# Optimization experiments

Measured on AMD Instinct MI355X. Metric: run time of the kernel, lower is better.

## Reference

```python
import jax, jax.numpy as jnp
import numpy as np

NUM_EMBED = 8192
EMBED_DIM = 256


def setup_inputs() -> dict:
    key = jax.random.key(0)
    k1, k2 = jax.random.split(key)
    input_data = jax.random.normal(k1, (32, EMBED_DIM, 32, 32), dtype=jnp.float32)
    codebook = jax.random.normal(k2, (NUM_EMBED, EMBED_DIM), dtype=jnp.float32)
    return {"input_data": input_data, "codebook": codebook}


def reference(input_data, codebook):
    N, C, H, W = input_data.shape
    # NCHW -> NHWC -> [N*H*W, C]
    data = jnp.transpose(input_data, (0, 2, 3, 1)).reshape(-1, C)
    dist = (
        jnp.sum(data * data, axis=1, keepdims=True)          # [T, 1]
        - 2.0 * jnp.einsum("tc,kc->tk", data, codebook)      # [T, K]
        + jnp.sum(codebook * codebook, axis=1)[None, :]       # [1, K]
    )
    embed_ind = jnp.argmin(dist, axis=1)                      # [T]
    quantize = codebook[embed_ind]                            # [T, C] gather
    quantize_detach = data + jax.lax.stop_gradient(quantize - data)
    return quantize, quantize_detach, data
```

## Files before the change

kernel.cpp:

```cpp
#include <hip/hip_runtime.h>
#include <stdint.h>


#define T_TOT 32768
#define K_TOT 8192
#define CD    256
#define SPLITS 4
#define NSPLIT 2048
#define MT    64
#define NTI   32

typedef _Float16 h8 __attribute__((ext_vector_type(8)));
typedef _Float16 h4 __attribute__((ext_vector_type(4)));
typedef float f4 __attribute__((ext_vector_type(4)));
typedef unsigned long long u64;
typedef unsigned int u32;

#define WS_AP    0u
#define WS_BP    16777216u
#define WS_E2    20971520u
#define WS_E2B   21004288u
#define WS_CAND  21037056u
#define WS_NEED  23265280u

__device__ __forceinline__ u64 shfl_xor_u64(u64 v, int off, int w) {
  unsigned lo = (unsigned)v, hi = (unsigned)(v >> 32);
  lo = __shfl_xor(lo, off, w);
  hi = __shfl_xor(hi, off, w);
  return ((u64)hi << 32) | lo;
}
__device__ __forceinline__ u64 umin64(u64 a, u64 b) { return a < b ? a : b; }
__device__ __forceinline__ u64 umax64(u64 a, u64 b) { return a < b ? b : a; }
__device__ __forceinline__ u32 umin32(u32 a, u32 b) { return a < b ? a : b; }
__device__ __forceinline__ u32 umax32(u32 a, u32 b) { return a < b ? b : a; }

__device__ __forceinline__ void gll16(const void* g, void* l) {
  __builtin_amdgcn_global_load_lds(
      (const __attribute__((address_space(1))) void*)g,
      (__attribute__((address_space(3))) void*)l, 16, 0, 0);
}

__device__ __forceinline__ void stage_b(const _Float16* __restrict__ gsrc,
                                        _Float16* ldst, int lane) {
  #pragma unroll
  for (int kk = 0; kk < 8; ++kk)
    gll16(gsrc + kk * 512 + lane * 8, ldst + kk * 512);
}



__global__ __launch_bounds__(256) void cvt_data_kernel(
    const float* __restrict__ in, _Float16* __restrict__ Ap) {
  __shared__ float Ds[32][257];
  const int tid = threadIdx.x;
  const int t0 = blockIdx.x * 32;
  const int nbase = (t0 >> 10) << 18;
  const int tin = t0 & 1023;
  #pragma unroll 8
  for (int p = 0; p < 32; ++p) {
    const int lin = p * 256 + tid;
    const int cc = lin >> 5, tt = lin & 31;
    Ds[tt][cc] = in[nbase + cc * 1024 + tin + tt];
  }
  __syncthreads();
  const u64 g0 = (u64)(t0 >> 4);
  #pragma unroll
  for (int p = 0; p < 4; ++p) {
    const int id = p * 256 + tid;
    const int gl = id >> 9, kk = (id >> 6) & 7, l = id & 63;
    const int row = gl * 16 + (l & 15);
    const int c0 = kk * 32 + (l >> 4) * 8;
    h8 hv;
    #pragma unroll
    for (int j = 0; j < 8; ++j) hv[j] = (_Float16)(-Ds[row][c0 + j]);
    *(h8*)(Ap + ((g0 + (u64)gl) * 8 + kk) * 512 + (u64)l * 8) = hv;
  }
}

__global__ __launch_bounds__(256) void cvt_cb_kernel(
    const float* __restrict__ cb, _Float16* __restrict__ Bp,
    float* __restrict__ e2, float* __restrict__ e2b) {
  __shared__ float Cs[16][260];
  const int tid = threadIdx.x;
  const int g = blockIdx.x;
  #pragma unroll
  for (int r = 0; r < 16; ++r)
    Cs[r][tid] = cb[((u64)g * 16 + r) * 256 + tid];
  __syncthreads();
  const int w = tid >> 6, lane = tid & 63;
  #pragma unroll
  for (int rr = 0; rr < 4; ++rr) {
    const int row = w * 4 + rr;
    const float4 v = *(const float4*)&Cs[row][lane * 4];
    float s = v.x * v.x + v.y * v.y + v.z * v.z + v.w * v.w;
    #pragma unroll
    for (int off = 32; off >= 1; off >>= 1) s += __shfl_xor(s, off, 64);
    if (lane == 0) {
      e2[g * 16 + row] = s;
      e2b[g * 16 + row] = 0.5f * s + 256.0f;
    }
  }
  #pragma unroll
  for (int p = 0; p < 2; ++p) {
    const int id = p * 256 + tid;
    const int kk = id >> 6, l = id & 63;
    const int row = l & 15, c0 = kk * 32 + (l >> 4) * 8;
    h8 hv;
    #pragma unroll
    for (int j = 0; j < 8; ++j) hv[j] = (_Float16)Cs[row][c0 + j];
    *(h8*)(Bp + ((u64)g * 8 + kk) * 512 + (u64)l * 8) = hv;
  }
}

__global__ __launch_bounds__(256, 2) void screen_kernel(
    const _Float16* __restrict__ Ap, const _Float16* __restrict__ Bp,
    const float* __restrict__ e2b, u64* __restrict__ cand) {
  __shared__ __align__(16) _Float16 bsm[4][2][4096];
  __shared__ __align__(16) float e2s[2048];

  const int tid = threadIdx.x;
  const int lane = tid & 63;
  const int w = __builtin_amdgcn_readfirstlane(tid >> 6);
  const int q = lane >> 4;
  const int c15 = lane & 15;

  const int x = blockIdx.x & 7;
  const int m = blockIdx.x >> 3;
  const int split = x >> 1;
  const int bm = m * 2 + (x & 1);
  const int t0 = bm * MT;
  const int n0s = split * NSPLIT;

  const h8* ap = (const h8*)Ap + (u64)(t0 >> 4) * 512 + lane;
  h8 af[4][8];
  #pragma unroll
  for (int mi = 0; mi < 4; ++mi)
    #pragma unroll
    for (int kk = 0; kk < 8; ++kk)
      af[mi][kk] = ap[(mi * 8 + kk) * 64];

  const _Float16* bg = Bp + ((u64)(n0s >> 4) + (u64)w) * 4096;
  stage_b(bg, &bsm[w][0][0], lane);
  stage_b(bg + 16384, &bsm[w][1][0], lane);
  gll16(e2b + n0s + w * 512 + lane * 4, e2s + w * 512);
  gll16(e2b + n0s + w * 512 + 256 + lane * 4, e2s + w * 512 + 256);

  u32 m1[16], m2[16];
  #pragma unroll
  for (int r = 0; r < 16; ++r) { m1[r] = 0xffffffffu; m2[r] = 0xffffffffu; }

  __syncthreads();

  #pragma unroll 2
  for (int nt = 0; nt < NTI; ++nt) {
    asm volatile("s_waitcnt vmcnt(8)" ::: "memory");
    _Float16* slot = &bsm[w][nt & 1][0];
    const float ev = e2s[nt * 64 + w * 16 + c15];
    h8 bf[8];
    #pragma unroll
    for (int kk = 0; kk < 8; ++kk)
      bf[kk] = *(const h8*)(slot + kk * 512 + lane * 8);

    f4 acc[4];
    #pragma unroll
    for (int mi = 0; mi < 4; ++mi) acc[mi] = (f4){ev, ev, ev, ev};
    __builtin_amdgcn_s_setprio(1);
    #pragma unroll
    for (int kk = 0; kk < 8; ++kk) {
      acc[0] = __builtin_amdgcn_mfma_f32_16x16x32_f16(af[0][kk], bf[kk], acc[0], 0, 0, 0);
      acc[1] = __builtin_amdgcn_mfma_f32_16x16x32_f16(af[1][kk], bf[kk], acc[1], 0, 0, 0);
      acc[2] = __builtin_amdgcn_mfma_f32_16x16x32_f16(af[2][kk], bf[kk], acc[2], 0, 0, 0);
      acc[3] = __builtin_amdgcn_mfma_f32_16x16x32_f16(af[3][kk], bf[kk], acc[3], 0, 0, 0);
    }
    __builtin_amdgcn_s_setprio(0);

    asm volatile("s_waitcnt lgkmcnt(0)" ::: "memory");
    __builtin_amdgcn_sched_barrier(0);
    const int g2 = (nt + 2 < NTI) ? nt + 2 : NTI - 1;
    stage_b(bg + (u64)g2 * 16384, slot, lane);

    #pragma unroll
    for (int mi = 0; mi < 4; ++mi)
      #pragma unroll
      for (int reg = 0; reg < 4; ++reg) {
        const int r = mi * 4 + reg;
        const u32 k = (__float_as_uint(acc[mi][reg]) & ~63u) | (u32)nt;
        const u32 hi = umax32(m1[r], k);
        m1[r] = umin32(m1[r], k);
        m2[r] = umin32(m2[r], hi);
      }
  }

  u64 P1[16], P2[16];
  #pragma unroll
  for (int r = 0; r < 16; ++r) {
    const u32 l1 = m1[r] & 63u, l2 = m2[r] & 63u;
    const u32 col1 = (u32)(n0s + (int)l1 * 64 + w * 16 + c15);
    const u32 col2 = (u32)(n0s + (int)l2 * 64 + w * 16 + c15);
    P1[r] = ((u64)m1[r] << 32) | col1;
    P2[r] = ((u64)m2[r] << 32) | col2;
  }
  #pragma unroll
  for (int st = 1; st < 16; st <<= 1) {
    #pragma unroll
    for (int r = 0; r < 16; ++r) {
      const u64 o1 = shfl_xor_u64(P1[r], st, 16);
      const u64 o2 = shfl_xor_u64(P2[r], st, 16);
      const u64 n1 = umin64(P1[r], o1);
      const u64 hi = umax64(P1[r], o1);
      P2[r] = umin64(hi, umin64(P2[r], o2));
      P1[r] = n1;
    }
  }
  __syncthreads();
  u64* mb = (u64*)&bsm[0][0][0];
  if (c15 == 0) {
    #pragma unroll
    for (int r = 0; r < 16; ++r) {
      const int mi = r >> 2, reg = r & 3;
      const int row = mi * 16 + q * 4 + reg;
      mb[(w * 64 + row) * 2 + 0] = P1[r];
      mb[(w * 64 + row) * 2 + 1] = P2[r];
    }
  }
  __syncthreads();
  if (tid < 64) {
    const u64 a1 = mb[(0 * 64 + tid) * 2], a2 = mb[(0 * 64 + tid) * 2 + 1];
    const u64 b1 = mb[(1 * 64 + tid) * 2], b2 = mb[(1 * 64 + tid) * 2 + 1];
    const u64 c1 = mb[(2 * 64 + tid) * 2], c2 = mb[(2 * 64 + tid) * 2 + 1];
    const u64 d1 = mb[(3 * 64 + tid) * 2], d2 = mb[(3 * 64 + tid) * 2 + 1];
    const u64 x1 = umin64(a1, b1);
    const u64 x2 = umin64(umax64(a1, b1), umin64(a2, b2));
    const u64 y1 = umin64(c1, d1);
    const u64 y2 = umin64(umax64(c1, d1), umin64(c2, d2));
    const u64 n1 = umin64(x1, y1);
    const u64 n2 = umin64(umax64(x1, y1), umin64(x2, y2));
    cand[(u64)(t0 + tid) * 8 + split * 2 + 0] = n1;
    cand[(u64)(t0 + tid) * 8 + split * 2 + 1] = n2;
  }
}

__global__ __launch_bounds__(256) void rescore_output_kernel(
    const float* __restrict__ in, const float* __restrict__ cb,
    const float* __restrict__ e2, const u64* __restrict__ cand,
    float* __restrict__ out) {
  __shared__ __align__(16) float Ds[32][260];
  __shared__ int idxs[32];
  const int tid = threadIdx.x;
  const int t0 = blockIdx.x * 32;
  const int nbase = (t0 >> 10) << 18;
  const int tin = t0 & 1023;
  #pragma unroll 8
  for (int p = 0; p < 32; ++p) {
    const int lin = p * 256 + tid;
    const int cc = lin >> 5, tt = lin & 31;
    Ds[tt][cc] = in[nbase + cc * 1024 + tin + tt];
  }
  __syncthreads();
  const int w = tid >> 6, lane = tid & 63;
  for (int s = 0; s < 8; ++s) {
    const int tt = w * 8 + s;
    const int t = t0 + tt;
    int colv = 0;
    if (lane < 8) colv = (int)(u32)cand[(u64)t * 8 + lane];
    const float4 x = *(const float4*)&Ds[tt][lane * 4];
    float bestd = 1e30f; int bestc = 0x7fffffff;
    #pragma unroll
    for (int j = 0; j < 8; ++j) {
      const int col = __shfl(colv, j, 64);
      const float4 e = *(const float4*)(cb + (u64)col * CD + lane * 4);
      float p4 = x.x * e.x + x.y * e.y + x.z * e.z + x.w * e.w;
      #pragma unroll
      for (int off = 32; off >= 1; off >>= 1) p4 += __shfl_xor(p4, off, 64);
      const float d = e2[col] - 2.0f * p4;
      if (d < bestd || (d == bestd && col < bestc)) { bestd = d; bestc = col; }
    }
    if (lane == 0) idxs[tt] = bestc;
  }
  __syncthreads();
  float* out1 = out;
  float* out2 = out + 8388608;
  float* out3 = out + 16777216;
  const int c4 = lane * 4;
  for (int s = 0; s < 8; ++s) {
    const int tt = w * 8 + s;
    const float4 d4 = *(const float4*)&Ds[tt][c4];
    const int k = idxs[tt];
    const float4 q4 = *(const float4*)(cb + (u64)k * CD + c4);
    float4 qd4;
    qd4.x = d4.x + (q4.x - d4.x);
    qd4.y = d4.y + (q4.y - d4.y);
    qd4.z = d4.z + (q4.z - d4.z);
    qd4.w = d4.w + (q4.w - d4.w);
    const int o = (t0 + tt) * CD + c4;
    *(float4*)(out1 + o) = q4;
    *(float4*)(out2 + o) = qd4;
    *(float4*)(out3 + o) = d4;
  }
}


__global__ __launch_bounds__(256) void norms_kernel(const float* __restrict__ in,
                                                    const float* __restrict__ cb,
                                                    float* __restrict__ e2,
                                                    float* __restrict__ x2) {
  const int b = blockIdx.x;
  const int tid = threadIdx.x;
  if (b < 2048) {
    const int wave = tid >> 6, lane = tid & 63;
    const int row = b * 4 + wave;
    const float4 v = *(const float4*)(cb + row * CD + lane * 4);
    float s = v.x * v.x + v.y * v.y + v.z * v.z + v.w * v.w;
    #pragma unroll
    for (int off = 32; off >= 1; off >>= 1) s += __shfl_down(s, off, 64);
    if (lane == 0) e2[row] = s;
  } else {
    const int t = (b - 2048) * 256 + tid;
    const float* p = in + ((t >> 10) << 18) + (t & 1023);
    float s = 0.f;
    #pragma unroll 8
    for (int c = 0; c < CD; ++c) { const float v = p[c << 10]; s += v * v; }
    x2[t] = s;
  }
}

__global__ __launch_bounds__(256) void dist_argmin_kernel(
    const float* __restrict__ in, const float* __restrict__ cb,
    const float* __restrict__ e2, const float* __restrict__ x2,
    u64* __restrict__ packed) {
  __shared__ __align__(16) float As_[32][128];
  __shared__ __align__(16) float Bs_[32][128];
  const int tid = threadIdx.x;
  const int tx = tid & 15, ty = tid >> 4;
  const int tb = blockIdx.x & 255;
  const int ks = blockIdx.x >> 8;
  const int t0 = tb * 128;
  const int nbase = (t0 >> 10) << 18;
  const int tin = t0 & 1023;
  float xi[8];
  #pragma unroll
  for (int i = 0; i < 8; ++i)
    xi[i] = x2[t0 + ty * 4 + (i & 3) + ((i >> 2) << 6)];
  u64 best[8];
  #pragma unroll
  for (int i = 0; i < 8; ++i) best[i] = ~0ull;
  for (int kt = 0; kt < 32; ++kt) {
    const int k0 = ks * 4096 + kt * 128;
    float acc[8][8];
    #pragma unroll
    for (int i = 0; i < 8; ++i)
      #pragma unroll
      for (int j = 0; j < 8; ++j) acc[i][j] = 0.f;
    float ej[8];
    #pragma unroll
    for (int j = 0; j < 8; ++j)
      ej[j] = e2[k0 + tx * 4 + (j & 3) + ((j >> 2) << 6)];
    for (int ch = 0; ch < 8; ++ch) {
      const int c0 = ch * 32;
      #pragma unroll
      for (int p = 0; p < 4; ++p) {
        const int l = p * 1024 + tid * 4;
        const int cc = l >> 7, tt = l & 127;
        *(float4*)&As_[cc][tt] =
            *(const float4*)(in + nbase + (c0 + cc) * 1024 + tin + tt);
      }
      #pragma unroll
      for (int p = 0; p < 4; ++p) {
        const int ix = p * 256 + tid;
        const int kk = ix >> 3, cs = (ix & 7) * 4;
        const float4 v = *(const float4*)(cb + (k0 + kk) * CD + c0 + cs);
        Bs_[cs + 0][kk] = v.x; Bs_[cs + 1][kk] = v.y;
        Bs_[cs + 2][kk] = v.z; Bs_[cs + 3][kk] = v.w;
      }
      __syncthreads();
      #pragma unroll
      for (int cc = 0; cc < 32; ++cc) {
        const float4 a0 = *(const float4*)&As_[cc][ty * 4];
        const float4 a1 = *(const float4*)&As_[cc][64 + ty * 4];
        const float4 b0 = *(const float4*)&Bs_[cc][tx * 4];
        const float4 b1 = *(const float4*)&Bs_[cc][64 + tx * 4];
        const float a[8]  = {a0.x, a0.y, a0.z, a0.w, a1.x, a1.y, a1.z, a1.w};
        const float bb[8] = {b0.x, b0.y, b0.z, b0.w, b1.x, b1.y, b1.z, b1.w};
        #pragma unroll
        for (int i = 0; i < 8; ++i)
          #pragma unroll
          for (int j = 0; j < 8; ++j)
            acc[i][j] += a[i] * bb[j];
      }
      __syncthreads();
    }
    #pragma unroll
    for (int i = 0; i < 8; ++i) {
      u64 m = best[i];
      #pragma unroll
      for (int j = 0; j < 8; ++j) {
        const float dist = (xi[i] - 2.0f * acc[i][j]) + ej[j];
        const int kidx = k0 + tx * 4 + (j & 3) + ((j >> 2) << 6);
        const u64 pk = ((u64)__float_as_uint(dist) << 32) | (unsigned)kidx;
        m = pk < m ? pk : m;
      }
      best[i] = m;
    }
  }
  #pragma unroll
  for (int i = 0; i < 8; ++i) {
    u64 m = best[i];
    #pragma unroll
    for (int off = 8; off >= 1; off >>= 1) {
      const u64 o = shfl_xor_u64(m, off, 16);
      m = o < m ? o : m;
    }
    if (tx == 0)
      atomicMin(&packed[t0 + ty * 4 + (i & 3) + ((i >> 2) << 6)], m);
  }
}

__global__ __launch_bounds__(256) void output_kernel(
    const float* __restrict__ in, const float* __restrict__ cb,
    const u64* __restrict__ packed, float* __restrict__ out) {
  __shared__ float Ds[32][257];
  __shared__ int idxs[32];
  const int tid = threadIdx.x;
  const int t0 = blockIdx.x * 32;
  const int nbase = (t0 >> 10) << 18;
  const int tin = t0 & 1023;
  if (tid < 32) idxs[tid] = (int)(packed[t0 + tid] & 0xffffffffull);
  #pragma unroll 8
  for (int p = 0; p < 32; ++p) {
    const int lin = p * 256 + tid;
    const int cc = lin >> 5, tt = lin & 31;
    Ds[tt][cc] = in[nbase + cc * 1024 + tin + tt];
  }
  __syncthreads();
  float* out1 = out;
  float* out2 = out + 8388608;
  float* out3 = out + 16777216;
  for (int tt = 0; tt < 32; ++tt) {
    const float d = Ds[tt][tid];
    const int k = idxs[tt];
    const float q = cb[k * CD + tid];
    const float qd = d + (q - d);
    const int o = (t0 + tt) * CD + tid;
    out1[o] = q;
    out2[o] = qd;
    out3[o] = d;
  }
}

extern "C" void kernel_launch(void* const* d_in, const int* in_sizes, int n_in,
                              void* d_out, int out_size, void* d_ws, size_t ws_size,
                              hipStream_t stream) {
  const float* in = (const float*)d_in[0];
  const float* cb = (const float*)d_in[1];
  float* out = (float*)d_out;

  if (ws_size >= WS_NEED) {
    _Float16* Ap = (_Float16*)((char*)d_ws + WS_AP);
    _Float16* Bp = (_Float16*)((char*)d_ws + WS_BP);
    float* e2  = (float*)((char*)d_ws + WS_E2);
    float* e2b = (float*)((char*)d_ws + WS_E2B);
    u64* cand  = (u64*)((char*)d_ws + WS_CAND);

    cvt_data_kernel<<<T_TOT / 32, 256, 0, stream>>>(in, Ap);
    cvt_cb_kernel<<<K_TOT / 16, 256, 0, stream>>>(cb, Bp, e2, e2b);
    screen_kernel<<<(T_TOT / MT) * SPLITS, 256, 0, stream>>>(Ap, Bp, e2b, cand);
    rescore_output_kernel<<<T_TOT / 32, 256, 0, stream>>>(in, cb, e2, cand, out);
  } else {
    u64* packed = (u64*)d_ws;
    float* e2 = (float*)((char*)d_ws + 262144);
    float* x2 = (float*)((char*)d_ws + 294912);
    (void)hipMemsetAsync(packed, 0xFF, T_TOT * sizeof(u64), stream);
    norms_kernel<<<2176, 256, 0, stream>>>(in, cb, e2, x2);
    dist_argmin_kernel<<<512, 256, 0, stream>>>(in, cb, e2, x2, packed);
    output_kernel<<<T_TOT / 32, 256, 0, stream>>>(in, cb, packed, out);
  }
}
```

Baseline: 333.5 us.

## Write transposed data output in conversion kernel and drop reload in rescore

The conversion kernel now loads the NCHW input with float4 reads and also writes the transposed NHWC data output from its shared-memory tile. The rescore/output kernel no longer re-reads and transposes the input through LDS. Instead it reads each token row back from that output buffer, and it fuses the argmin with the quantize writes so no intermediate LDS index array or barrier is needed. This removes a second strided transpose pass over the input, at the cost of re-reading the output buffer and moving its writes earlier in the pipeline.

```diff
diff --git a/kernel.cpp b/kernel.cpp
--- a/kernel.cpp
+++ b/kernel.cpp
@@ -50,17 +50,22 @@
 
 
 __global__ __launch_bounds__(256) void cvt_data_kernel(
-    const float* __restrict__ in, _Float16* __restrict__ Ap) {
+    const float* __restrict__ in, _Float16* __restrict__ Ap,
+    float* __restrict__ out3) {
   __shared__ float Ds[32][257];
   const int tid = threadIdx.x;
   const int t0 = blockIdx.x * 32;
   const int nbase = (t0 >> 10) << 18;
   const int tin = t0 & 1023;
-  #pragma unroll 8
-  for (int p = 0; p < 32; ++p) {
-    const int lin = p * 256 + tid;
-    const int cc = lin >> 5, tt = lin & 31;
-    Ds[tt][cc] = in[nbase + cc * 1024 + tin + tt];
+  #pragma unroll
+  for (int p = 0; p < 8; ++p) {
+    const int id = p * 256 + tid;
+    const int cc = id >> 3, t4 = (id & 7) * 4;
+    const float4 v = *(const float4*)(in + nbase + cc * 1024 + tin + t4);
+    Ds[t4 + 0][cc] = v.x;
+    Ds[t4 + 1][cc] = v.y;
+    Ds[t4 + 2][cc] = v.z;
+    Ds[t4 + 3][cc] = v.w;
   }
   __syncthreads();
   const u64 g0 = (u64)(t0 >> 4);
@@ -75,6 +80,9 @@
     for (int j = 0; j < 8; ++j) hv[j] = (_Float16)(-Ds[row][c0 + j]);
     *(h8*)(Ap + ((g0 + (u64)gl) * 8 + kk) * 512 + (u64)l * 8) = hv;
   }
+  #pragma unroll 8
+  for (int tt = 0; tt < 32; ++tt)
+    out3[(u64)(t0 + tt) * CD + tid] = Ds[tt][tid];
 }
 
 __global__ __launch_bounds__(256) void cvt_cb_kernel(
@@ -241,29 +249,20 @@
 }
 
 __global__ __launch_bounds__(256) void rescore_output_kernel(
-    const float* __restrict__ in, const float* __restrict__ cb,
-    const float* __restrict__ e2, const u64* __restrict__ cand,
-    float* __restrict__ out) {
-  __shared__ __align__(16) float Ds[32][260];
-  __shared__ int idxs[32];
-  const int tid = threadIdx.x;
-  const int t0 = blockIdx.x * 32;
-  const int nbase = (t0 >> 10) << 18;
-  const int tin = t0 & 1023;
-  #pragma unroll 8
-  for (int p = 0; p < 32; ++p) {
-    const int lin = p * 256 + tid;
-    const int cc = lin >> 5, tt = lin & 31;
-    Ds[tt][cc] = in[nbase + cc * 1024 + tin + tt];
-  }
-  __syncthreads();
+    const float* __restrict__ cb, const float* __restrict__ e2,
+    const u64* __restrict__ cand, float* __restrict__ out) {
+  const int tid = threadIdx.x;
   const int w = tid >> 6, lane = tid & 63;
+  const int t0 = blockIdx.x * 32 + w * 8;
+  float* out1 = out;
+  float* out2 = out + 8388608;
+  const float* out3 = out + 16777216;
+  #pragma unroll 1
   for (int s = 0; s < 8; ++s) {
-    const int tt = w * 8 + s;
-    const int t = t0 + tt;
+    const int t = t0 + s;
     int colv = 0;
     if (lane < 8) colv = (int)(u32)cand[(u64)t * 8 + lane];
-    const float4 x = *(const float4*)&Ds[tt][lane * 4];
+    const float4 x = *(const float4*)(out3 + (u64)t * CD + lane * 4);
     float bestd = 1e30f; int bestc = 0x7fffffff;
     #pragma unroll
     for (int j = 0; j < 8; ++j) {
@@ -275,27 +274,15 @@
       const float d = e2[col] - 2.0f * p4;
       if (d < bestd || (d == bestd && col < bestc)) { bestd = d; bestc = col; }
     }
-    if (lane == 0) idxs[tt] = bestc;
-  }
-  __syncthreads();
-  float* out1 = out;
-  float* out2 = out + 8388608;
-  float* out3 = out + 16777216;
-  const int c4 = lane * 4;
-  for (int s = 0; s < 8; ++s) {
-    const int tt = w * 8 + s;
-    const float4 d4 = *(const float4*)&Ds[tt][c4];
-    const int k = idxs[tt];
-    const float4 q4 = *(const float4*)(cb + (u64)k * CD + c4);
+    const float4 q4 = *(const float4*)(cb + (u64)bestc * CD + lane * 4);
     float4 qd4;
-    qd4.x = d4.x + (q4.x - d4.x);
-    qd4.y = d4.y + (q4.y - d4.y);
-    qd4.z = d4.z + (q4.z - d4.z);
-    qd4.w = d4.w + (q4.w - d4.w);
-    const int o = (t0 + tt) * CD + c4;
+    qd4.x = x.x + (q4.x - x.x);
+    qd4.y = x.y + (q4.y - x.y);
+    qd4.z = x.z + (q4.z - x.z);
+    qd4.w = x.w + (q4.w - x.w);
+    const u64 o = (u64)t * CD + lane * 4;
     *(float4*)(out1 + o) = q4;
     *(float4*)(out2 + o) = qd4;
-    *(float4*)(out3 + o) = d4;
   }
 }
 
@@ -460,11 +447,12 @@
     float* e2  = (float*)((char*)d_ws + WS_E2);
     float* e2b = (float*)((char*)d_ws + WS_E2B);
     u64* cand  = (u64*)((char*)d_ws + WS_CAND);
-
-    cvt_data_kernel<<<T_TOT / 32, 256, 0, stream>>>(in, Ap);
+    float* out3 = out + 16777216;
+
+    cvt_data_kernel<<<T_TOT / 32, 256, 0, stream>>>(in, Ap, out3);
     cvt_cb_kernel<<<K_TOT / 16, 256, 0, stream>>>(cb, Bp, e2, e2b);
     screen_kernel<<<(T_TOT / MT) * SPLITS, 256, 0, stream>>>(Ap, Bp, e2b, cand);
-    rescore_output_kernel<<<T_TOT / 32, 256, 0, stream>>>(in, cb, e2, cand, out);
+    rescore_output_kernel<<<T_TOT / 32, 256, 0, stream>>>(cb, e2, cand, out);
   } else {
     u64* packed = (u64*)d_ws;
     float* e2 = (float*)((char*)d_ws + 262144);
```

After: 329.7 us. Within noise of the previous version (-1.1%).
